# Kernel optimization log

Hardware: AMD Instinct MI355X
Metric: run time of the kernel (lower is better)

## Reference

```python
import jax, jax.numpy as jnp
import numpy as np

N = 100000      # nodes
E = 1250000     # edges
D_IN = 64
D_OUT = 64


def _gconv(x, src, dst, W_rel, W_root, b, n_nodes):
    # PyG GraphConv (aggr='add'): out = lin_rel(sum_{j in N(i)} x_j) + lin_root(x_i)
    agg = jax.ops.segment_sum(x[src], dst, num_segments=n_nodes)  # [N, d]
    return agg @ W_rel + b + x @ W_root


def setup_inputs() -> dict:
    key = jax.random.key(0)
    ks = jax.random.split(key, 12)
    graph = jax.random.normal(ks[0], (N, D_IN), dtype=jnp.float32)
    edge_index = jax.random.randint(ks[1], (2, E), 0, N, dtype=jnp.int32)
    s_in = 1.0 / np.sqrt(D_IN)
    s_out = 1.0 / np.sqrt(D_OUT)
    d = {
        "graph": graph,
        "edge_index": edge_index,
        "W1_rel": jax.random.uniform(ks[2], (D_IN, D_OUT), jnp.float32, -s_in, s_in),
        "W1_root": jax.random.uniform(ks[3], (D_IN, D_OUT), jnp.float32, -s_in, s_in),
        "b1": jnp.zeros((D_OUT,), jnp.float32),
        "W2_rel": jax.random.uniform(ks[4], (D_OUT, D_OUT), jnp.float32, -s_out, s_out),
        "W2_root": jax.random.uniform(ks[5], (D_OUT, D_OUT), jnp.float32, -s_out, s_out),
        "b2": jnp.zeros((D_OUT,), jnp.float32),
        "W3_rel": jax.random.uniform(ks[6], (D_OUT, D_OUT), jnp.float32, -s_out, s_out),
        "W3_root": jax.random.uniform(ks[7], (D_OUT, D_OUT), jnp.float32, -s_out, s_out),
        "b3": jnp.zeros((D_OUT,), jnp.float32),
    }
    return d


def reference(graph, edge_index, W1_rel, W1_root, b1, W2_rel, W2_root, b2, W3_rel, W3_root, b3):
    src, dst = edge_index[0], edge_index[1]
    n = graph.shape[0]
    y1 = jax.nn.elu(_gconv(graph, src, dst, W1_rel, W1_root, b1, n))
    y2 = jax.nn.elu(_gconv(y1, src, dst, W2_rel, W2_root, b2, n))
    y3 = jax.nn.sigmoid(_gconv(y2, src, dst, W3_rel, W3_root, b3, n))
    return (y1, y2, y3)
```

## Files before the change

### kernel.cpp

```cpp
#include <hip/hip_runtime.h>
#include <hip/hip_bf16.h>
#include <math.h>


#define D 64
#define BSHIFT 9
#define BW 512
#define BCAP 8192

typedef __attribute__((ext_vector_type(8))) short short8;
typedef __attribute__((ext_vector_type(4))) float f32x4;

__device__ __forceinline__ ushort f2b(float f) {
    uint x = __float_as_uint(f);
    uint r = (x + 0x7fffu + ((x >> 16) & 1u)) >> 16;
    return (ushort)r;
}
__device__ __forceinline__ float b2f(ushort u) {
    return __uint_as_float(((uint)u) << 16);
}


__global__ __launch_bounds__(256) void convert_w(const float* __restrict__ w0,
                                                 const float* __restrict__ w1,
                                                 const float* __restrict__ w2,
                                                 const float* __restrict__ w3,
                                                 const float* __restrict__ w4,
                                                 const float* __restrict__ w5,
                                                 ushort* __restrict__ out,
                                                 int* __restrict__ bucketCnt) {
    if (blockIdx.x == 0 && threadIdx.x < 256) bucketCnt[threadIdx.x] = 0;
    int m = blockIdx.x >> 4;
    int t = (blockIdx.x & 15) * 256 + threadIdx.x;
    const float* src = m == 0 ? w0 : m == 1 ? w1 : m == 2 ? w2 : m == 3 ? w3 : m == 4 ? w4 : w5;
    int k = t >> 6, d = t & 63;
    out[m * 4096 + d * 64 + k] = f2b(src[t]);
}


__global__ __launch_bounds__(1024) void bucket_scatter(const int* __restrict__ src,
                                                       const int* __restrict__ dst,
                                                       int* __restrict__ bucketCnt,
                                                       unsigned long long* __restrict__ store,
                                                       int E) {
    __shared__ int h[256], base[256], cur[256];
    int t = threadIdx.x;
    if (t < 256) { h[t] = 0; cur[t] = 0; }
    __syncthreads();
    int e = blockIdx.x * 1024 + t;
    int s = 0, d = 0, b = 0;
    bool ok = e < E;
    if (ok) {
        s = src[e];
        d = dst[e];
        b = d >> BSHIFT;
        atomicAdd(&h[b], 1);
    }
    __syncthreads();
    if (t < 256) base[t] = h[t] ? atomicAdd(&bucketCnt[t], h[t]) : 0;
    __syncthreads();
    if (ok) {
        int r = atomicAdd(&cur[b], 1);
        int pos = base[b] + r;
        if (pos < BCAP)
            store[(size_t)b * BCAP + pos] = ((unsigned long long)(uint)d << 32) | (uint)s;
    }
}


__global__ __launch_bounds__(256) void scan_buckets(const int* __restrict__ bucketCnt,
                                                    int* __restrict__ bucketBase,
                                                    int* __restrict__ offs,
                                                    int nb, int n, int E) {
    __shared__ int tmp[256];
    int t = threadIdx.x;
    int v = (t < nb) ? bucketCnt[t] : 0;
    tmp[t] = v;
    __syncthreads();
    for (int off = 1; off < 256; off <<= 1) {
        int add = (t >= off) ? tmp[t - off] : 0;
        __syncthreads();
        tmp[t] += add;
        __syncthreads();
    }
    if (t < nb) bucketBase[t] = tmp[t] - v;
    if (t == 0) offs[n] = E;
}


__global__ __launch_bounds__(1024) void bucket_build(const int* __restrict__ bucketCnt,
                                                     const int* __restrict__ bucketBase,
                                                     const unsigned long long* __restrict__ store,
                                                     int* __restrict__ offs,
                                                     int* __restrict__ src_sorted, int n) {
    __shared__ int h[BW], loc[BW], cur[BW];
    __shared__ unsigned long long se[BCAP];
    int b = blockIdx.x, t = threadIdx.x;
    int cnt = bucketCnt[b];
    if (cnt > BCAP) cnt = BCAP;
    int obase = bucketBase[b];
    int d0 = b << BSHIFT;
    int nd = n - d0;
    if (nd > BW) nd = BW;
    if (t < BW) { h[t] = 0; cur[t] = 0; }
    __syncthreads();
    for (int i = t; i < cnt; i += 1024) {
        unsigned long long p = store[(size_t)b * BCAP + i];
        se[i] = p;
        atomicAdd(&h[(int)(p >> 32) - d0], 1);
    }
    __syncthreads();
    if (t < BW) loc[t] = h[t];
    __syncthreads();
    for (int off = 1; off < BW; off <<= 1) {
        int add = (t < BW && t >= off) ? loc[t - off] : 0;
        __syncthreads();
        if (t < BW) loc[t] += add;
        __syncthreads();
    }
    if (t < nd) offs[d0 + t] = obase + loc[t] - h[t];
    __syncthreads();
    for (int i = t; i < cnt; i += 1024) {
        unsigned long long p = se[i];
        int dl = (int)(p >> 32) - d0;
        int r = atomicAdd(&cur[dl], 1);
        src_sorted[obase + loc[dl] - h[dl] + r] = (int)(p & 0xffffffffULL);
    }
}


__global__ __launch_bounds__(256) void gemm_ro(const float* __restrict__ x,
                                               const ushort* __restrict__ WtR,
                                               const ushort* __restrict__ WtO,
                                               const float* __restrict__ bias,
                                               ushort* __restrict__ hrel,
                                               ushort* __restrict__ hroot, int n) {
    __shared__ ushort hsR[4][16 * 64];
    __shared__ ushort hsO[4][16 * 64];
    int t = threadIdx.x;
    int w = t >> 6, l = t & 63;
    int i0 = blockIdx.x * 64 + w * 16;
    int lr = l & 15, kb = l >> 4;
    int row = i0 + lr;
    int rowc = row < n ? row : n - 1;

    short8 a[2];
#pragma unroll
    for (int s = 0; s < 2; ++s) {
        const float* p = x + (size_t)rowc * D + s * 32 + kb * 8;
        float4 u = *(const float4*)p;
        float4 v = *(const float4*)(p + 4);
        a[s][0] = f2b(u.x); a[s][1] = f2b(u.y); a[s][2] = f2b(u.z); a[s][3] = f2b(u.w);
        a[s][4] = f2b(v.x); a[s][5] = f2b(v.y); a[s][6] = f2b(v.z); a[s][7] = f2b(v.w);
    }

#pragma unroll
    for (int ct = 0; ct < 4; ++ct) {
        f32x4 accR = (f32x4){0.f, 0.f, 0.f, 0.f};
        f32x4 accO = (f32x4){0.f, 0.f, 0.f, 0.f};
#pragma unroll
        for (int s = 0; s < 2; ++s) {
            short8 bR = *(const short8*)(WtR + (ct * 16 + lr) * D + s * 32 + kb * 8);
            short8 bO = *(const short8*)(WtO + (ct * 16 + lr) * D + s * 32 + kb * 8);
            accR = __builtin_amdgcn_mfma_f32_16x16x32_bf16(a[s], bR, accR, 0, 0, 0);
            accO = __builtin_amdgcn_mfma_f32_16x16x32_bf16(a[s], bO, accO, 0, 0, 0);
        }
        float bv = bias[ct * 16 + lr];
#pragma unroll
        for (int i = 0; i < 4; ++i) {
            hsR[w][(kb * 4 + i) * 64 + ct * 16 + lr] = f2b(accR[i]);
            hsO[w][(kb * 4 + i) * 64 + ct * 16 + lr] = f2b(accO[i] + bv);
        }
    }
    __syncthreads();

    int r = l >> 2, ch = l & 3;
    int grow = i0 + r;
    if (grow < n) {
        const float4* spR = (const float4*)&hsR[w][r * 64 + ch * 16];
        const float4* spO = (const float4*)&hsO[w][r * 64 + ch * 16];
        float4 r0 = spR[0];
        float4 r1 = spR[1];
        float4 o0 = spO[0];
        float4 o1 = spO[1];
        *(float4*)(hrel + (size_t)grow * D + ch * 16) = r0;
        *(float4*)(hrel + (size_t)grow * D + ch * 16 + 8) = r1;
        *(float4*)(hroot + (size_t)grow * D + ch * 16) = o0;
        *(float4*)(hroot + (size_t)grow * D + ch * 16 + 8) = o1;
    }
}


template <int ACT>
__global__ __launch_bounds__(256) void agg_act(const ushort* __restrict__ hrel,
                                               const ushort* __restrict__ hroot,
                                               const int* __restrict__ offs,
                                               const int* __restrict__ srcs,
                                               float* __restrict__ y, int n) {
    int node = blockIdx.x * 4 + (threadIdx.x >> 6);
    int l = threadIdx.x & 63;
    if (node >= n) return;
    int q = l >> 4, r = l & 15;
    int beg = offs[node];
    int end = offs[node + 1];

    float a0 = 0.f, a1 = 0.f, a2 = 0.f, a3 = 0.f;
    for (int e0 = beg; e0 < end; e0 += 16) {
#pragma unroll
        for (int k = 0; k < 4; ++k) {
            int ee = e0 + k * 4 + q;
            int eec = ee < end ? ee : end - 1;
            int s = srcs[eec];
            uint2 u = *(const uint2*)(hrel + (size_t)s * D + r * 4);
            float m = (ee < end) ? 1.f : 0.f;
            a0 = fmaf(__uint_as_float(u.x << 16), m, a0);
            a1 = fmaf(__uint_as_float(u.x & 0xffff0000u), m, a1);
            a2 = fmaf(__uint_as_float(u.y << 16), m, a2);
            a3 = fmaf(__uint_as_float(u.y & 0xffff0000u), m, a3);
        }
    }

    a0 += __shfl_xor(a0, 32); a0 += __shfl_xor(a0, 16);
    a1 += __shfl_xor(a1, 32); a1 += __shfl_xor(a1, 16);
    a2 += __shfl_xor(a2, 32); a2 += __shfl_xor(a2, 16);
    a3 += __shfl_xor(a3, 32); a3 += __shfl_xor(a3, 16);

    uint2 hr = *(const uint2*)(hroot + (size_t)node * D + r * 4);
    a0 += __uint_as_float(hr.x << 16);
    a1 += __uint_as_float(hr.x & 0xffff0000u);
    a2 += __uint_as_float(hr.y << 16);
    a3 += __uint_as_float(hr.y & 0xffff0000u);

    if (ACT == 0) {
        a0 = a0 > 0.f ? a0 : __expf(a0) - 1.f;
        a1 = a1 > 0.f ? a1 : __expf(a1) - 1.f;
        a2 = a2 > 0.f ? a2 : __expf(a2) - 1.f;
        a3 = a3 > 0.f ? a3 : __expf(a3) - 1.f;
    } else {
        a0 = __builtin_amdgcn_rcpf(1.f + __expf(-a0));
        a1 = __builtin_amdgcn_rcpf(1.f + __expf(-a1));
        a2 = __builtin_amdgcn_rcpf(1.f + __expf(-a2));
        a3 = __builtin_amdgcn_rcpf(1.f + __expf(-a3));
    }

    if (q == 0) {
        float4 o; o.x = a0; o.y = a1; o.z = a2; o.w = a3;
        *(float4*)(y + (size_t)node * D + r * 4) = o;
    }
}


extern "C" void kernel_launch(void* const* d_in, const int* in_sizes, int n_in,
                              void* d_out, int out_size, void* d_ws, size_t ws_size,
                              hipStream_t stream) {
    const float* graph = (const float*)d_in[0];
    const int* eidx    = (const int*)d_in[1];
    const float* W1r = (const float*)d_in[2];
    const float* W1o = (const float*)d_in[3];
    const float* b1  = (const float*)d_in[4];
    const float* W2r = (const float*)d_in[5];
    const float* W2o = (const float*)d_in[6];
    const float* b2  = (const float*)d_in[7];
    const float* W3r = (const float*)d_in[8];
    const float* W3o = (const float*)d_in[9];
    const float* b3  = (const float*)d_in[10];

    int n = in_sizes[0] / D;
    int E = in_sizes[1] / 2;
    const int* src  = eidx;
    const int* dstl = eidx + E;
    int nb = (n + BW - 1) >> BSHIFT;

    char* w = (char*)d_ws;
    auto carve = [&](size_t bytes) {
        void* p = (void*)w;
        w += (bytes + 255) & ~(size_t)255;
        return p;
    };
    ushort* hrel  = (ushort*)carve((size_t)n * D * sizeof(ushort));
    ushort* hroot = (ushort*)carve((size_t)n * D * sizeof(ushort));
    unsigned long long* store = (unsigned long long*)hrel;
    int* offs       = (int*)carve((size_t)(n + 1) * sizeof(int));
    int* src_sorted = (int*)carve((size_t)E * sizeof(int));
    int* bucketCnt  = (int*)carve(256 * sizeof(int));
    int* bucketBase = (int*)carve(256 * sizeof(int));
    ushort* wt      = (ushort*)carve(6 * 4096 * sizeof(ushort));
    ushort* wtR1 = wt;
    ushort* wtO1 = wt + 1 * 4096;
    ushort* wtR2 = wt + 2 * 4096;
    ushort* wtO2 = wt + 3 * 4096;
    ushort* wtR3 = wt + 4 * 4096;
    ushort* wtO3 = wt + 5 * 4096;

    int eb1 = (E + 1023) / 1024;
    int tb  = (n + 63) / 64;
    int ab  = (n + 3) / 4;

    convert_w<<<96, 256, 0, stream>>>(W1r, W1o, W2r, W2o, W3r, W3o, wt, bucketCnt);
    bucket_scatter<<<eb1, 1024, 0, stream>>>(src, dstl, bucketCnt, store, E);
    scan_buckets<<<1, 256, 0, stream>>>(bucketCnt, bucketBase, offs, nb, n, E);
    bucket_build<<<nb, 1024, 0, stream>>>(bucketCnt, bucketBase, store, offs, src_sorted, n);

    float* out = (float*)d_out;
    float* y1 = out;
    float* y2 = out + (size_t)n * D;
    float* y3 = out + 2 * (size_t)n * D;

    gemm_ro<<<tb, 256, 0, stream>>>(graph, wtR1, wtO1, b1, hrel, hroot, n);
    agg_act<0><<<ab, 256, 0, stream>>>(hrel, hroot, offs, src_sorted, y1, n);
    gemm_ro<<<tb, 256, 0, stream>>>(y1, wtR2, wtO2, b2, hrel, hroot, n);
    agg_act<0><<<ab, 256, 0, stream>>>(hrel, hroot, offs, src_sorted, y2, n);
    gemm_ro<<<tb, 256, 0, stream>>>(y2, wtR3, wtO3, b3, hrel, hroot, n);
    agg_act<1><<<ab, 256, 0, stream>>>(hrel, hroot, offs, src_sorted, y3, n);
}
```

Measured before the change: 315.1 us.

## Pack edge records into 32 bits and process two nodes per wave in aggregation

Bucket records shrink from 64-bit (dst,src) pairs to 32-bit words holding the local destination in the high bits and a 17-bit source index. This halves scatter and build traffic and the shared-memory footprint. The aggregation kernel now has each wave walk two destination nodes' edge lists together, which gives more independent gathers in flight. Inactive lanes read a zero padding row instead of using a clamp-and-mask FMA. The 17-bit packing only holds for node counts up to 131072, which narrows generality.

```diff
diff --git a/kernel.cpp b/kernel.cpp
--- a/kernel.cpp
+++ b/kernel.cpp
@@ -15,9 +15,6 @@
     uint x = __float_as_uint(f);
     uint r = (x + 0x7fffu + ((x >> 16) & 1u)) >> 16;
     return (ushort)r;
-}
-__device__ __forceinline__ float b2f(ushort u) {
-    return __uint_as_float(((uint)u) << 16);
 }
 
 
@@ -28,8 +25,10 @@
                                                  const float* __restrict__ w4,
                                                  const float* __restrict__ w5,
                                                  ushort* __restrict__ out,
-                                                 int* __restrict__ bucketCnt) {
+                                                 int* __restrict__ bucketCnt,
+                                                 ushort* __restrict__ hrel_zrow) {
     if (blockIdx.x == 0 && threadIdx.x < 256) bucketCnt[threadIdx.x] = 0;
+    if (blockIdx.x == 1 && threadIdx.x < 32) ((uint*)hrel_zrow)[threadIdx.x] = 0;
     int m = blockIdx.x >> 4;
     int t = (blockIdx.x & 15) * 256 + threadIdx.x;
     const float* src = m == 0 ? w0 : m == 1 ? w1 : m == 2 ? w2 : m == 3 ? w3 : m == 4 ? w4 : w5;
@@ -41,19 +40,20 @@
 __global__ __launch_bounds__(1024) void bucket_scatter(const int* __restrict__ src,
                                                        const int* __restrict__ dst,
                                                        int* __restrict__ bucketCnt,
-                                                       unsigned long long* __restrict__ store,
+                                                       uint* __restrict__ store,
                                                        int E) {
     __shared__ int h[256], base[256], cur[256];
     int t = threadIdx.x;
     if (t < 256) { h[t] = 0; cur[t] = 0; }
     __syncthreads();
     int e = blockIdx.x * 1024 + t;
-    int s = 0, d = 0, b = 0;
+    uint rec = 0; int b = 0;
     bool ok = e < E;
     if (ok) {
-        s = src[e];
-        d = dst[e];
+        int s = src[e];
+        int d = dst[e];
         b = d >> BSHIFT;
+        rec = ((uint)(d & (BW - 1)) << 17) | (uint)s;
         atomicAdd(&h[b], 1);
     }
     __syncthreads();
@@ -63,7 +63,7 @@
         int r = atomicAdd(&cur[b], 1);
         int pos = base[b] + r;
         if (pos < BCAP)
-            store[(size_t)b * BCAP + pos] = ((unsigned long long)(uint)d << 32) | (uint)s;
+            store[(size_t)b * BCAP + pos] = rec;
     }
 }
 
@@ -90,11 +90,11 @@
 
 __global__ __launch_bounds__(1024) void bucket_build(const int* __restrict__ bucketCnt,
                                                      const int* __restrict__ bucketBase,
-                                                     const unsigned long long* __restrict__ store,
+                                                     const uint* __restrict__ store,
                                                      int* __restrict__ offs,
                                                      int* __restrict__ src_sorted, int n) {
     __shared__ int h[BW], loc[BW], cur[BW];
-    __shared__ unsigned long long se[BCAP];
+    __shared__ uint se[BCAP];
     int b = blockIdx.x, t = threadIdx.x;
     int cnt = bucketCnt[b];
     if (cnt > BCAP) cnt = BCAP;
@@ -105,9 +105,9 @@
     if (t < BW) { h[t] = 0; cur[t] = 0; }
     __syncthreads();
     for (int i = t; i < cnt; i += 1024) {
-        unsigned long long p = store[(size_t)b * BCAP + i];
+        uint p = store[(size_t)b * BCAP + i];
         se[i] = p;
-        atomicAdd(&h[(int)(p >> 32) - d0], 1);
+        atomicAdd(&h[p >> 17], 1);
     }
     __syncthreads();
     if (t < BW) loc[t] = h[t];
@@ -121,10 +121,10 @@
     if (t < nd) offs[d0 + t] = obase + loc[t] - h[t];
     __syncthreads();
     for (int i = t; i < cnt; i += 1024) {
-        unsigned long long p = se[i];
-        int dl = (int)(p >> 32) - d0;
+        uint p = se[i];
+        int dl = p >> 17;
         int r = atomicAdd(&cur[dl], 1);
-        src_sorted[obase + loc[dl] - h[dl] + r] = (int)(p & 0xffffffffULL);
+        src_sorted[obase + loc[dl] - h[dl] + r] = (int)(p & 0x1FFFFu);
     }
 }
 
@@ -197,54 +197,74 @@
                                                const int* __restrict__ offs,
                                                const int* __restrict__ srcs,
                                                float* __restrict__ y, int n) {
-    int node = blockIdx.x * 4 + (threadIdx.x >> 6);
+    int nA = blockIdx.x * 8 + (threadIdx.x >> 6) * 2;
     int l = threadIdx.x & 63;
-    if (node >= n) return;
+    if (nA >= n) return;
+    int nB = nA + 1;
+    bool hasB = nB < n;
     int q = l >> 4, r = l & 15;
-    int beg = offs[node];
-    int end = offs[node + 1];
+
+    int oA = offs[nA];
+    int oB = offs[nA + 1];
+    int oC = hasB ? offs[nA + 2] : oB;
 
     float a0 = 0.f, a1 = 0.f, a2 = 0.f, a3 = 0.f;
-    for (int e0 = beg; e0 < end; e0 += 16) {
+    float b0 = 0.f, b1 = 0.f, b2 = 0.f, b3 = 0.f;
+
+    int eA = oA, eB = oB;
+    while (eA < oB || eB < oC) {
 #pragma unroll
         for (int k = 0; k < 4; ++k) {
-            int ee = e0 + k * 4 + q;
-            int eec = ee < end ? ee : end - 1;
-            int s = srcs[eec];
-            uint2 u = *(const uint2*)(hrel + (size_t)s * D + r * 4);
-            float m = (ee < end) ? 1.f : 0.f;
-            a0 = fmaf(__uint_as_float(u.x << 16), m, a0);
-            a1 = fmaf(__uint_as_float(u.x & 0xffff0000u), m, a1);
-            a2 = fmaf(__uint_as_float(u.y << 16), m, a2);
-            a3 = fmaf(__uint_as_float(u.y & 0xffff0000u), m, a3);
+            int ia = eA + k * 4 + q;
+            int ib = eB + k * 4 + q;
+            int sA = (ia < oB) ? srcs[ia] : n;
+            int sB = (ib < oC) ? srcs[ib] : n;
+            uint2 uA = *(const uint2*)(hrel + (size_t)sA * D + r * 4);
+            uint2 uB = *(const uint2*)(hrel + (size_t)sB * D + r * 4);
+            a0 += __uint_as_float(uA.x << 16);
+            a1 += __uint_as_float(uA.x & 0xffff0000u);
+            a2 += __uint_as_float(uA.y << 16);
+            a3 += __uint_as_float(uA.y & 0xffff0000u);
+            b0 += __uint_as_float(uB.x << 16);
+            b1 += __uint_as_float(uB.x & 0xffff0000u);
+            b2 += __uint_as_float(uB.y << 16);
+            b3 += __uint_as_float(uB.y & 0xffff0000u);
         }
+        eA += 16; eB += 16;
     }
 
     a0 += __shfl_xor(a0, 32); a0 += __shfl_xor(a0, 16);
     a1 += __shfl_xor(a1, 32); a1 += __shfl_xor(a1, 16);
     a2 += __shfl_xor(a2, 32); a2 += __shfl_xor(a2, 16);
     a3 += __shfl_xor(a3, 32); a3 += __shfl_xor(a3, 16);
-
-    uint2 hr = *(const uint2*)(hroot + (size_t)node * D + r * 4);
-    a0 += __uint_as_float(hr.x << 16);
-    a1 += __uint_as_float(hr.x & 0xffff0000u);
-    a2 += __uint_as_float(hr.y << 16);
-    a3 += __uint_as_float(hr.y & 0xffff0000u);
-
-    if (ACT == 0) {
-        a0 = a0 > 0.f ? a0 : __expf(a0) - 1.f;
-        a1 = a1 > 0.f ? a1 : __expf(a1) - 1.f;
-        a2 = a2 > 0.f ? a2 : __expf(a2) - 1.f;
-        a3 = a3 > 0.f ? a3 : __expf(a3) - 1.f;
-    } else {
-        a0 = __builtin_amdgcn_rcpf(1.f + __expf(-a0));
-        a1 = __builtin_amdgcn_rcpf(1.f + __expf(-a1));
-        a2 = __builtin_amdgcn_rcpf(1.f + __expf(-a2));
-        a3 = __builtin_amdgcn_rcpf(1.f + __expf(-a3));
-    }
-
-    if (q == 0) {
-        float4 o; o.x = a0; o.y = a1; o.z = a2; o.w = a3;
+    b0 += __shfl_xor(b0, 32); b0 += __shfl_xor(b0, 16);
+    b1 += __shfl_xor(b1, 32); b1 += __shfl_xor(b1, 16);
+    b2 += __shfl_xor(b2, 32); b2 += __shfl_xor(b2, 16);
+    b3 += __shfl_xor(b3, 32); b3 += __shfl_xor(b3, 16);
+
+    if (q < 2 && (q == 0 || hasB)) {
+        int node = q == 0 ? nA : nB;
+        float v0 = q == 0 ? a0 : b0;
+        float v1 = q == 0 ? a1 : b1;
+        float v2 = q == 0 ? a2 : b2;
+        float v3 = q == 0 ? a3 : b3;
+        uint2 hr = *(const uint2*)(hroot + (size_t)node * D + r * 4);
+        v0 += __uint_as_float(hr.x << 16);
+        v1 += __uint_as_float(hr.x & 0xffff0000u);
+        v2 += __uint_as_float(hr.y << 16);
+        v3 += __uint_as_float(hr.y & 0xffff0000u);
+        if (ACT == 0) {
+            v0 = v0 > 0.f ? v0 : __expf(v0) - 1.f;
+            v1 = v1 > 0.f ? v1 : __expf(v1) - 1.f;
+            v2 = v2 > 0.f ? v2 : __expf(v2) - 1.f;
+            v3 = v3 > 0.f ? v3 : __expf(v3) - 1.f;
+        } else {
+            v0 = __builtin_amdgcn_rcpf(1.f + __expf(-v0));
+            v1 = __builtin_amdgcn_rcpf(1.f + __expf(-v1));
+            v2 = __builtin_amdgcn_rcpf(1.f + __expf(-v2));
+            v3 = __builtin_amdgcn_rcpf(1.f + __expf(-v3));
+        }
+        float4 o; o.x = v0; o.y = v1; o.z = v2; o.w = v3;
         *(float4*)(y + (size_t)node * D + r * 4) = o;
     }
 }
@@ -277,11 +297,11 @@
         w += (bytes + 255) & ~(size_t)255;
         return p;
     };
-    ushort* hrel  = (ushort*)carve((size_t)n * D * sizeof(ushort));
+    ushort* hrel  = (ushort*)carve((size_t)(n + 1) * D * sizeof(ushort));
     ushort* hroot = (ushort*)carve((size_t)n * D * sizeof(ushort));
-    unsigned long long* store = (unsigned long long*)hrel;
+    uint* store = (uint*)hrel;
     int* offs       = (int*)carve((size_t)(n + 1) * sizeof(int));
-    int* src_sorted = (int*)carve((size_t)E * sizeof(int));
+    int* src_sorted = (int*)carve((size_t)(E + 16) * sizeof(int));
     int* bucketCnt  = (int*)carve(256 * sizeof(int));
     int* bucketBase = (int*)carve(256 * sizeof(int));
     ushort* wt      = (ushort*)carve(6 * 4096 * sizeof(ushort));
@@ -294,9 +314,10 @@
 
     int eb1 = (E + 1023) / 1024;
     int tb  = (n + 63) / 64;
-    int ab  = (n + 3) / 4;
-
-    convert_w<<<96, 256, 0, stream>>>(W1r, W1o, W2r, W2o, W3r, W3o, wt, bucketCnt);
+    int ab  = (n + 7) / 8;
+
+    convert_w<<<96, 256, 0, stream>>>(W1r, W1o, W2r, W2o, W3r, W3o, wt, bucketCnt,
+                                      hrel + (size_t)n * D);
     bucket_scatter<<<eb1, 1024, 0, stream>>>(src, dstl, bucketCnt, store, E);
     scan_buckets<<<1, 256, 0, stream>>>(bucketCnt, bucketBase, offs, nb, n, E);
     bucket_build<<<nb, 1024, 0, stream>>>(bucketCnt, bucketBase, store, offs, src_sorted, n);
@@ -305,6 +326,7 @@
     float* y1 = out;
     float* y2 = out + (size_t)n * D;
     float* y3 = out + 2 * (size_t)n * D;
+
 
     gemm_ro<<<tb, 256, 0, stream>>>(graph, wtR1, wtO1, b1, hrel, hroot, n);
     agg_act<0><<<ab, 256, 0, stream>>>(hrel, hroot, offs, src_sorted, y1, n);
```

New measurement: 316.5 us. Within noise of the previous version (+0.4%).
